# Kernel tuning notes

Hardware: AMD Instinct MI355X
Metric: run time of the kernel (lower is better)

Reference implementation:

```python
import jax, jax.numpy as jnp
import numpy as np

B, N, FDIM = 8, 2048, 256
ASSIGN_RATIO = 0.1
K = int(N * ASSIGN_RATIO) + 1  # num coarse nodes per graph (205)
DENSITY = 0.01


def setup_inputs() -> dict:
    key = jax.random.key(0)
    k1, k2, k3 = jax.random.split(key, 3)
    x = jax.random.normal(k1, (B, N, FDIM), dtype=jnp.float32)
    u = jax.random.uniform(k2, (B, N, N), dtype=jnp.float32)
    adj = jnp.where(u < DENSITY, u, 0.0)
    adj = 0.5 * (adj + jnp.swapaxes(adj, 1, 2))  # symmetric weighted adjacency
    W = jax.random.normal(k3, (FDIM, 1), dtype=jnp.float32) * 0.05
    b = jnp.zeros((1,), dtype=jnp.float32)
    return {"x": x, "adj": adj, "W": W, "b": b}


def _coarsen(x, adj, W, b):
    I = jnp.eye(N, dtype=adj.dtype)
    # --- GCNConv attention score (self-loops + symmetric normalization) ---
    A_hat = adj + I                       # [B,N,N]
    dg = A_hat.sum(-1) ** -0.5            # deg >= 1 via self-loop
    gcn_norm = dg[:, :, None] * A_hat * dg[:, None, :]
    alpha = jnp.einsum('bnm,bmf,fo->bno', gcn_norm, x, W) + b
    alpha = jax.nn.sigmoid(alpha ** 2)[..., 0]   # [B,N], sigmoid(gcn^2)
    # --- normalize_batch_adj: D^{-1/2}(A+I)D^{-1/2}, zero isolated rows ---
    d = jnp.clip(A_hat.sum(-1), 1.0, None) ** -0.5
    norm_adj = d[:, :, None] * A_hat * d[:, None, :]
    norm_adj = norm_adj * (adj.sum(-1) > 0).astype(adj.dtype)[:, :, None]
    # --- top-k cut on attention ---
    topv, topi = jax.lax.top_k(alpha, K)  # [B,K]
    cut = topv[:, K - 1]                  # k-th largest value per graph
    cut_alpha = jax.nn.relu(alpha + 1e-7 - cut[:, None])   # [B,N]
    # --- assignment matrix S = L1-row-normalized(norm_adj * cut_alpha_cols) ---
    S = norm_adj * cut_alpha[:, None, :]
    S = S / jnp.clip(jnp.abs(S).sum(-1, keepdims=True), 1e-12, None)
    # --- coarsening matmuls ---
    x_c = jnp.einsum('bnm,bnf->bmf', S, x)                 # S^T x
    coarse = jnp.einsum('bnm,bnk,bkl->bml', S, adj, S)     # S^T A S
    coarse = jnp.floor(coarse * 1e4) / 1e4                 # 4-digit truncation
    return x_c, coarse, S, topi


def reference(x, adj, W, b):
    return _coarsen(x, adj, W, b)
```

## Files before the change

kernel.cpp:

```cpp
#include <hip/hip_runtime.h>
#include <cstdint>
#include <cstddef>

#define BB 8
#define NN 2048
#define FD 256
#define KK 205
#define CAP 96
#define SELCAP 256

typedef float f4 __attribute__((ext_vector_type(4)));


__global__ __launch_bounds__(256) void k_spy(const float* __restrict__ adj, const float* __restrict__ x,
                                             const float* __restrict__ W, int2* __restrict__ ell,
                                             int* __restrict__ ell_cnt, float* __restrict__ dg,
                                             float* __restrict__ dgy) {
  int r = blockIdx.x;
  const f4* arow4 = (const f4*)(adj + (size_t)r * NN);
  int t = threadIdx.x;
  int lane = t & 63, wv = t >> 6;
  __shared__ int counter;
  __shared__ float wsum[4], wy[4];
  if (t == 0) counter = 0;
  __syncthreads();
  size_t base = (size_t)r * CAP;
  unsigned long long lmask = (1ull << lane) - 1;
  float ls = 0.f;
#pragma unroll
  for (int j = 0; j < 2; ++j) {
    int i4 = t + j * 256;
    f4 v = __builtin_nontemporal_load(&arow4[i4]);
    int m0 = i4 * 4;
#pragma unroll
    for (int c = 0; c < 4; ++c) {
      float val = v[c];
      unsigned long long mk = __ballot(val != 0.f);
      if (mk) {
        int wbase = 0;
        if (lane == 0) wbase = atomicAdd(&counter, (int)__popcll(mk));
        wbase = __shfl(wbase, 0);
        if (val != 0.f) {
          int p = wbase + (int)__popcll(mk & lmask);
          if (p < CAP) ell[base + p] = make_int2(m0 + c, __float_as_int(val));
        }
      }
      ls += val;
    }
  }
#pragma unroll
  for (int off = 32; off > 0; off >>= 1) ls += __shfl_down(ls, off);
  if (lane == 0) wsum[wv] = ls;
  float xv = x[(size_t)r * FD + t] * W[t];
#pragma unroll
  for (int off = 32; off > 0; off >>= 1) xv += __shfl_down(xv, off);
  if (lane == 0) wy[wv] = xv;
  __syncthreads();
  if (t == 0) {
    int tot = counter; if (tot > CAP) tot = CAP;
    ell_cnt[r] = tot;
    float rs = wsum[0] + wsum[1] + wsum[2] + wsum[3];
    float d = 1.0f / sqrtf(1.0f + rs);
    dg[r] = d;
    dgy[r] = d * (wy[0] + wy[1] + wy[2] + wy[3]);
  }
}

__global__ __launch_bounds__(256) void k_alpha(const int2* __restrict__ ell, const int* __restrict__ ell_cnt,
                                               const float* __restrict__ dg, const float* __restrict__ dgy,
                                               const float* __restrict__ bptr, float* __restrict__ alpha) {
  int lane = threadIdx.x & 63, wv = threadIdx.x >> 6;
  int r = blockIdx.x * 4 + wv;
  int b = r / NN;
  int cnt = ell_cnt[r];
  size_t base = (size_t)r * CAP;
  const float* gyb = dgy + (size_t)b * NN;
  float acc = 0.f;
  for (int j = lane; j < cnt; j += 64) {
    int2 e = ell[base + j];
    acc += __int_as_float(e.y) * gyb[e.x];
  }
#pragma unroll
  for (int off = 32; off > 0; off >>= 1) acc += __shfl_down(acc, off);
  if (lane == 0) {
    float dgn = dg[r];
    float z = dgn * (acc + dgy[r]) + bptr[0];
    float t2 = z * z;
    alpha[r] = 1.0f / (1.0f + expf(-t2));
  }
}

__global__ __launch_bounds__(256) void k_rank(const float* __restrict__ alpha, float* __restrict__ cutv,
                                              float* __restrict__ out_topi, int* __restrict__ sel_cnt) {
  __shared__ unsigned int keys[NN];
  int b = blockIdx.x & 7;
  int chunk = blockIdx.x >> 3;
  int t = threadIdx.x;
  if (chunk == 0 && t == 0) sel_cnt[b] = 0;
  const float* ab = alpha + (size_t)b * NN;
  for (int i = t; i < NN; i += 256) keys[i] = __float_as_uint(ab[i]);
  __syncthreads();
  int i = chunk * 256 + t;
  unsigned int ai = keys[i];
  int rank = 0;
  const uint4* k4 = (const uint4*)keys;
#pragma unroll 4
  for (int j4 = 0; j4 < NN / 4; ++j4) {
    uint4 v = k4[j4];
    int j = j4 * 4;
    rank += (v.x > ai) || (v.x == ai && (j + 0) < i);
    rank += (v.y > ai) || (v.y == ai && (j + 1) < i);
    rank += (v.z > ai) || (v.z == ai && (j + 2) < i);
    rank += (v.w > ai) || (v.w == ai && (j + 3) < i);
  }
  if (rank < KK) out_topi[(size_t)b * KK + rank] = (float)i;
  if (rank == KK - 1) cutv[b] = __uint_as_float(ai);
}

__global__ __launch_bounds__(256) void k_selcut(const float* __restrict__ alpha, const float* __restrict__ cutv,
                                                const float* __restrict__ dg, int2* __restrict__ seldg,
                                                int* __restrict__ sel_list, int* __restrict__ sel_cnt) {
  int r = blockIdx.x * 256 + threadIdx.x;
  int b = r / NN, n = r % NN;
  float ca = fmaxf(alpha[r] + 1e-7f - cutv[b], 0.0f);
  int s = -1;
  if (ca > 0.f) {
    s = atomicAdd(&sel_cnt[b], 1);
    if (s < SELCAP) sel_list[b * SELCAP + s] = n; else s = -1;
  }
  seldg[r] = make_int2(__float_as_int(dg[r] * ca), s);
}

__global__ __launch_bounds__(256) void k_sbuild(const int2* __restrict__ ell, const int* __restrict__ ell_cnt,
                                                const float* __restrict__ dg, const int2* __restrict__ seldg,
                                                const int* __restrict__ sel_cnt,
                                                float* __restrict__ dginv,
                                                float* __restrict__ Sc, float* __restrict__ outS) {
  __shared__ float row[NN];
  __shared__ float scrow[SELCAP];
  __shared__ int   sidx[CAP];
  __shared__ int   ssel[CAP];
  __shared__ float sterm[CAP];
  __shared__ float wred[4];
  int r = blockIdx.x;
  int b = r >> 11;
  int n = r & (NN - 1);
  int t = threadIdx.x;
  int lane = t & 63, wv = t >> 6;
#pragma unroll
  for (int j = 0; j < NN / 256; ++j) row[t + j * 256] = 0.f;
  if (t < SELCAP) scrow[t] = 0.f;
  int cnt = ell_cnt[r];
  size_t base = (size_t)r * CAP;
  float dgn = dg[r];
  const int2* sdb = seldg + (size_t)b * NN;
  float part = 0.f;
  for (int j = t; j < cnt; j += 256) {
    int2 e = ell[base + j];
    int2 sd = sdb[e.x];
    float term = dgn * __int_as_float(e.y) * __int_as_float(sd.x);
    sidx[j] = e.x; ssel[j] = sd.y; sterm[j] = term;
    part += term;
  }
#pragma unroll
  for (int off = 32; off > 0; off >>= 1) part += __shfl_down(part, off);
  if (lane == 0) wred[wv] = part;
  __syncthreads();
  int2 sdn = sdb[n];
  float diag = dgn * __int_as_float(sdn.x);
  float rho = wred[0] + wred[1] + wred[2] + wred[3] + diag;
  float inv = (cnt > 0) ? (1.0f / fmaxf(rho, 1e-12f)) : 0.f;
  float dv = diag * inv;
  if (t == 0) dginv[r] = dgn * inv;
  for (int j = t; j < cnt; j += 256) {
    float v = sterm[j] * inv;
    row[sidx[j]] = v;
    int si = ssel[j];
    if (si >= 0) scrow[si] = v;
  }
  __syncthreads();
  int nsel = sel_cnt[b]; if (nsel > SELCAP) nsel = SELCAP;
  f4* dst = (f4*)(outS + (size_t)r * NN);
  const f4* src = (const f4*)row;
#pragma unroll
  for (int j = 0; j < NN / 4 / 256; ++j) {
    int idx = t + j * 256;
    f4 v = src[idx];
    int b4 = idx * 4;
    v[0] += (b4 + 0 == n) ? dv : 0.f;
    v[1] += (b4 + 1 == n) ? dv : 0.f;
    v[2] += (b4 + 2 == n) ? dv : 0.f;
    v[3] += (b4 + 3 == n) ? dv : 0.f;
    __builtin_nontemporal_store(v, &dst[idx]);
  }
  if (t < nsel) {
    float sv = scrow[t];
    if (t == sdn.y) sv += dv;
    Sc[(size_t)r * SELCAP + t] = sv;
  }
}

__global__ __launch_bounds__(256) void k_M(const int2* __restrict__ ell, const int* __restrict__ ell_cnt,
                                           const int* __restrict__ sel_cnt,
                                           const float* __restrict__ Sc, float* __restrict__ Mmat) {
  int b = blockIdx.x & 7;
  int n = blockIdx.x >> 3;
  int r = b * NN + n;
  int t = threadIdx.x;
  __shared__ int srk[CAP];
  __shared__ float sav[CAP];
  int cnt = ell_cnt[r];
  size_t base = (size_t)r * CAP;
  for (int e = t; e < cnt; e += 256) {
    int2 p = ell[base + e];
    srk[e] = b * NN + p.x;
    sav[e] = __int_as_float(p.y);
  }
  __syncthreads();
  int nsel = sel_cnt[b]; if (nsel > SELCAP) nsel = SELCAP;
  if (t >= nsel) return;
  float a0 = 0.f, a1 = 0.f, a2 = 0.f, a3 = 0.f, a4 = 0.f, a5 = 0.f, a6 = 0.f, a7 = 0.f;
  int e = 0;
  for (; e + 8 <= cnt; e += 8) {
    a0 += sav[e + 0] * Sc[(size_t)srk[e + 0] * SELCAP + t];
    a1 += sav[e + 1] * Sc[(size_t)srk[e + 1] * SELCAP + t];
    a2 += sav[e + 2] * Sc[(size_t)srk[e + 2] * SELCAP + t];
    a3 += sav[e + 3] * Sc[(size_t)srk[e + 3] * SELCAP + t];
    a4 += sav[e + 4] * Sc[(size_t)srk[e + 4] * SELCAP + t];
    a5 += sav[e + 5] * Sc[(size_t)srk[e + 5] * SELCAP + t];
    a6 += sav[e + 6] * Sc[(size_t)srk[e + 6] * SELCAP + t];
    a7 += sav[e + 7] * Sc[(size_t)srk[e + 7] * SELCAP + t];
  }
  for (; e < cnt; ++e) a0 += sav[e] * Sc[(size_t)srk[e] * SELCAP + t];
  Mmat[(size_t)r * SELCAP + t] = ((a0 + a1) + (a2 + a3)) + ((a4 + a5) + (a6 + a7));
}

__global__ __launch_bounds__(256) void k_epi2(const float* __restrict__ x, const int2* __restrict__ ell,
                                              const int* __restrict__ ell_cnt, const int2* __restrict__ seldg,
                                              const float* __restrict__ dginv, const int* __restrict__ sel_list,
                                              const int* __restrict__ sel_cnt, const float* __restrict__ Mmat,
                                              float* __restrict__ xc, float* __restrict__ coarse) {
  int b = blockIdx.x & 7;
  int m = blockIdx.x >> 3;
  int rm = b * NN + m;
  int t = threadIdx.x;
  __shared__ float row[NN];
  __shared__ int cn[CAP + 1];
  __shared__ float cw[CAP + 1];
  int2 sd_m = seldg[rm];
  bool sel = sd_m.y >= 0;
  if (!sel) {
    f4 z = (f4)(0.f);
    if (t < FD / 4) __builtin_nontemporal_store(z, &((f4*)(xc + (size_t)rm * FD))[t]);
    f4* dco = (f4*)(coarse + (size_t)rm * NN);
    __builtin_nontemporal_store(z, &dco[t]);
    __builtin_nontemporal_store(z, &dco[t + 256]);
    return;
  }
  int nsel = sel_cnt[b]; if (nsel > SELCAP) nsel = SELCAP;
  int cnt = ell_cnt[rm];
#pragma unroll
  for (int j = 0; j < NN / 256; ++j) row[t + j * 256] = 0.f;
  {
    float dgca_m = __int_as_float(sd_m.x);
    for (int j = t; j <= cnt; j += 256) {
      if (j < cnt) {
        int2 e = ell[(size_t)rm * CAP + j];
        cn[j] = b * NN + e.x;
        cw[j] = __int_as_float(e.y) * dgca_m * dginv[b * NN + e.x];
      } else {
        cn[j] = rm;
        cw[j] = dgca_m * dginv[rm];
      }
    }
  }
  __syncthreads();
  bool act = t < nsel;
  float axc = 0.f, aco = 0.f;
  int tot = cnt + 1;
  int e = 0;
  for (; e + 4 <= tot; e += 4) {
    int r0 = cn[e + 0], r1 = cn[e + 1], r2 = cn[e + 2], r3 = cn[e + 3];
    float w0 = cw[e + 0], w1 = cw[e + 1], w2 = cw[e + 2], w3 = cw[e + 3];
    float x0 = x[(size_t)r0 * FD + t];
    float x1 = x[(size_t)r1 * FD + t];
    float x2 = x[(size_t)r2 * FD + t];
    float x3 = x[(size_t)r3 * FD + t];
    float m0 = 0.f, m1 = 0.f, m2 = 0.f, m3 = 0.f;
    if (act) {
      m0 = Mmat[(size_t)r0 * SELCAP + t];
      m1 = Mmat[(size_t)r1 * SELCAP + t];
      m2 = Mmat[(size_t)r2 * SELCAP + t];
      m3 = Mmat[(size_t)r3 * SELCAP + t];
    }
    axc += w0 * x0 + w1 * x1 + w2 * x2 + w3 * x3;
    aco += w0 * m0 + w1 * m1 + w2 * m2 + w3 * m3;
  }
  for (; e < tot; ++e) {
    int rn = cn[e];
    float w = cw[e];
    axc += w * x[(size_t)rn * FD + t];
    if (act) aco += w * Mmat[(size_t)rn * SELCAP + t];
  }
  if (act) row[sel_list[b * SELCAP + t]] = floorf(aco * 10000.0f) / 10000.0f;
  __builtin_nontemporal_store(axc, &xc[(size_t)rm * FD + t]);
  __syncthreads();
  f4* dst = (f4*)(coarse + (size_t)rm * NN);
  const f4* src = (const f4*)row;
#pragma unroll
  for (int j = 0; j < NN / 4 / 256; ++j)
    __builtin_nontemporal_store(src[t + j * 256], &dst[t + j * 256]);
}

extern "C" void kernel_launch(void* const* d_in, const int* in_sizes, int n_in,
                              void* d_out, int out_size, void* d_ws, size_t ws_size,
                              hipStream_t stream) {
  (void)in_sizes; (void)n_in; (void)ws_size; (void)out_size;
  const float* x = (const float*)d_in[0];
  const float* adj = (const float*)d_in[1];
  const float* W = (const float*)d_in[2];
  const float* bptr = (const float*)d_in[3];

  float* out = (float*)d_out;
  const size_t XC_SZ = (size_t)BB * NN * FD;
  const size_t CO_SZ = (size_t)BB * NN * NN;
  const size_t S_SZ  = (size_t)BB * NN * NN;
  float* out_xc = out;
  float* out_co = out + XC_SZ;
  float* out_S  = out + XC_SZ + CO_SZ;
  float* out_ti = out + XC_SZ + CO_SZ + S_SZ;

  char* w = (char*)d_ws;
  int2*  ell     = (int2*)w;  w += (size_t)BB * NN * CAP * 8;
  float* Sc      = (float*)w; w += (size_t)BB * NN * SELCAP * 4;
  float* Mmat    = (float*)w; w += (size_t)BB * NN * SELCAP * 4;
  int2*  seldg   = (int2*)w;  w += (size_t)BB * NN * 8;
  int*   ell_cnt = (int*)w;   w += (size_t)BB * NN * 4;
  float* dg      = (float*)w; w += (size_t)BB * NN * 4;
  float* dgy     = (float*)w; w += (size_t)BB * NN * 4;
  float* alpha   = (float*)w; w += (size_t)BB * NN * 4;
  float* dginv   = (float*)w; w += (size_t)BB * NN * 4;
  float* cutv    = (float*)w; w += (size_t)BB * 4;
  int*   sel_cnt = (int*)w;   w += (size_t)BB * 4;
  int*   sel_list= (int*)w;   w += (size_t)BB * SELCAP * 4;

  k_spy<<<BB * NN, 256, 0, stream>>>(adj, x, W, ell, ell_cnt, dg, dgy);
  k_alpha<<<BB * NN / 4, 256, 0, stream>>>(ell, ell_cnt, dg, dgy, bptr, alpha);
  k_rank<<<BB * 8, 256, 0, stream>>>(alpha, cutv, out_ti, sel_cnt);
  k_selcut<<<BB * NN / 256, 256, 0, stream>>>(alpha, cutv, dg, seldg, sel_list, sel_cnt);
  k_sbuild<<<BB * NN, 256, 0, stream>>>(ell, ell_cnt, dg, seldg, sel_cnt, dginv, Sc, out_S);
  k_M<<<BB * NN, 256, 0, stream>>>(ell, ell_cnt, sel_cnt, Sc, Mmat);
  k_epi2<<<BB * NN, 256, 0, stream>>>(x, ell, ell_cnt, seldg, dginv,
                                      sel_list, sel_cnt, Mmat, out_xc, out_co);
}
```

Baseline: 517.0 us.

## Split compact-S build into wave-per-row kernel and fuse dense S write into M kernel

The old S-build kernel did two jobs in one 256-thread block per row: building the compact selected-column row Sc and writing the dense 2048-wide S row. The new small kernel builds only Sc, with one wavefront per row and a shuffle reduction instead of block-wide barriers. The dense S write now happens inside the M kernel, which recomputes each row value from dginv and the ELL entries it already loads. This moves the heavy dense store so it overlaps with M's gather work and cuts barriers and launch width in the Sc build, at the cost of redundant ELL and seldg reads and the assumption that a row's nonzero count fits in 128.

```diff
diff --git a/kernel.cpp b/kernel.cpp
--- a/kernel.cpp
+++ b/kernel.cpp
@@ -131,55 +131,81 @@
   seldg[r] = make_int2(__float_as_int(dg[r] * ca), s);
 }
 
-__global__ __launch_bounds__(256) void k_sbuild(const int2* __restrict__ ell, const int* __restrict__ ell_cnt,
-                                                const float* __restrict__ dg, const int2* __restrict__ seldg,
-                                                const int* __restrict__ sel_cnt,
-                                                float* __restrict__ dginv,
-                                                float* __restrict__ Sc, float* __restrict__ outS) {
-  __shared__ float row[NN];
-  __shared__ float scrow[SELCAP];
-  __shared__ int   sidx[CAP];
-  __shared__ int   ssel[CAP];
-  __shared__ float sterm[CAP];
-  __shared__ float wred[4];
-  int r = blockIdx.x;
-  int b = r >> 11;
-  int n = r & (NN - 1);
-  int t = threadIdx.x;
-  int lane = t & 63, wv = t >> 6;
-#pragma unroll
-  for (int j = 0; j < NN / 256; ++j) row[t + j * 256] = 0.f;
-  if (t < SELCAP) scrow[t] = 0.f;
+__global__ __launch_bounds__(256) void k_sc(const int2* __restrict__ ell, const int* __restrict__ ell_cnt,
+                                            const float* __restrict__ dg, const int2* __restrict__ seldg,
+                                            const int* __restrict__ sel_cnt,
+                                            float* __restrict__ dginv, float* __restrict__ Sc) {
+  int lane = threadIdx.x & 63, wv = threadIdx.x >> 6;
+  int r = blockIdx.x * 4 + wv;
+  int b = r >> 11, n = r & (NN - 1);
+  __shared__ float scrow[4][SELCAP];
+  float* sc = scrow[wv];
+#pragma unroll
+  for (int j = lane; j < SELCAP; j += 64) sc[j] = 0.f;
   int cnt = ell_cnt[r];
   size_t base = (size_t)r * CAP;
   float dgn = dg[r];
   const int2* sdb = seldg + (size_t)b * NN;
-  float part = 0.f;
-  for (int j = t; j < cnt; j += 256) {
-    int2 e = ell[base + j];
+  float t0 = 0.f, t1 = 0.f;
+  int s0 = -1, s1 = -1;
+  if (lane < cnt) {
+    int2 e = ell[base + lane];
     int2 sd = sdb[e.x];
-    float term = dgn * __int_as_float(e.y) * __int_as_float(sd.x);
-    sidx[j] = e.x; ssel[j] = sd.y; sterm[j] = term;
-    part += term;
-  }
+    t0 = dgn * __int_as_float(e.y) * __int_as_float(sd.x);
+    s0 = sd.y;
+  }
+  if (lane + 64 < cnt) {
+    int2 e = ell[base + lane + 64];
+    int2 sd = sdb[e.x];
+    t1 = dgn * __int_as_float(e.y) * __int_as_float(sd.x);
+    s1 = sd.y;
+  }
+  float part = t0 + t1;
 #pragma unroll
   for (int off = 32; off > 0; off >>= 1) part += __shfl_down(part, off);
-  if (lane == 0) wred[wv] = part;
-  __syncthreads();
+  part = __shfl(part, 0);
   int2 sdn = sdb[n];
   float diag = dgn * __int_as_float(sdn.x);
-  float rho = wred[0] + wred[1] + wred[2] + wred[3] + diag;
+  float rho = part + diag;
   float inv = (cnt > 0) ? (1.0f / fmaxf(rho, 1e-12f)) : 0.f;
+  if (lane == 0) dginv[r] = dgn * inv;
+  if (s0 >= 0) sc[s0] = t0 * inv;
+  if (s1 >= 0) sc[s1] = t1 * inv;
+  int nsel = sel_cnt[b]; if (nsel > SELCAP) nsel = SELCAP;
   float dv = diag * inv;
-  if (t == 0) dginv[r] = dgn * inv;
-  for (int j = t; j < cnt; j += 256) {
-    float v = sterm[j] * inv;
-    row[sidx[j]] = v;
-    int si = ssel[j];
-    if (si >= 0) scrow[si] = v;
-  }
-  __syncthreads();
-  int nsel = sel_cnt[b]; if (nsel > SELCAP) nsel = SELCAP;
+  for (int p = lane; p < nsel; p += 64) {
+    float sv = sc[p];
+    if (p == sdn.y) sv += dv;
+    Sc[(size_t)r * SELCAP + p] = sv;
+  }
+}
+
+__global__ __launch_bounds__(256) void k_Ms(const int2* __restrict__ ell, const int* __restrict__ ell_cnt,
+                                            const int* __restrict__ sel_cnt, const int2* __restrict__ seldg,
+                                            const float* __restrict__ dginv, const float* __restrict__ Sc,
+                                            float* __restrict__ Mmat, float* __restrict__ outS) {
+  int b = blockIdx.x & 7;
+  int n = blockIdx.x >> 3;
+  int r = b * NN + n;
+  int t = threadIdx.x;
+  __shared__ float row[NN];
+  __shared__ int srk[CAP];
+  __shared__ float sav[CAP];
+#pragma unroll
+  for (int j = 0; j < NN / 256; ++j) row[t + j * 256] = 0.f;
+  int cnt = ell_cnt[r];
+  size_t base = (size_t)r * CAP;
+  float dinv = dginv[r];
+  const int2* sdb = seldg + (size_t)b * NN;
+  for (int e = t; e < cnt; e += 256) {
+    int2 p = ell[base + e];
+    srk[e] = b * NN + p.x;
+    float v = __int_as_float(p.y);
+    sav[e] = v;
+    row[p.x] = dinv * v * __int_as_float(sdb[p.x].x);
+  }
+  __syncthreads();
+  float dv = dinv * __int_as_float(sdb[n].x);
   f4* dst = (f4*)(outS + (size_t)r * NN);
   const f4* src = (const f4*)row;
 #pragma unroll
@@ -193,30 +219,6 @@
     v[3] += (b4 + 3 == n) ? dv : 0.f;
     __builtin_nontemporal_store(v, &dst[idx]);
   }
-  if (t < nsel) {
-    float sv = scrow[t];
-    if (t == sdn.y) sv += dv;
-    Sc[(size_t)r * SELCAP + t] = sv;
-  }
-}
-
-__global__ __launch_bounds__(256) void k_M(const int2* __restrict__ ell, const int* __restrict__ ell_cnt,
-                                           const int* __restrict__ sel_cnt,
-                                           const float* __restrict__ Sc, float* __restrict__ Mmat) {
-  int b = blockIdx.x & 7;
-  int n = blockIdx.x >> 3;
-  int r = b * NN + n;
-  int t = threadIdx.x;
-  __shared__ int srk[CAP];
-  __shared__ float sav[CAP];
-  int cnt = ell_cnt[r];
-  size_t base = (size_t)r * CAP;
-  for (int e = t; e < cnt; e += 256) {
-    int2 p = ell[base + e];
-    srk[e] = b * NN + p.x;
-    sav[e] = __int_as_float(p.y);
-  }
-  __syncthreads();
   int nsel = sel_cnt[b]; if (nsel > SELCAP) nsel = SELCAP;
   if (t >= nsel) return;
   float a0 = 0.f, a1 = 0.f, a2 = 0.f, a3 = 0.f, a4 = 0.f, a5 = 0.f, a6 = 0.f, a7 = 0.f;
@@ -348,8 +350,8 @@
   k_alpha<<<BB * NN / 4, 256, 0, stream>>>(ell, ell_cnt, dg, dgy, bptr, alpha);
   k_rank<<<BB * 8, 256, 0, stream>>>(alpha, cutv, out_ti, sel_cnt);
   k_selcut<<<BB * NN / 256, 256, 0, stream>>>(alpha, cutv, dg, seldg, sel_list, sel_cnt);
-  k_sbuild<<<BB * NN, 256, 0, stream>>>(ell, ell_cnt, dg, seldg, sel_cnt, dginv, Sc, out_S);
-  k_M<<<BB * NN, 256, 0, stream>>>(ell, ell_cnt, sel_cnt, Sc, Mmat);
+  k_sc<<<BB * NN / 4, 256, 0, stream>>>(ell, ell_cnt, dg, seldg, sel_cnt, dginv, Sc);
+  k_Ms<<<BB * NN, 256, 0, stream>>>(ell, ell_cnt, sel_cnt, seldg, dginv, Sc, Mmat, out_S);
   k_epi2<<<BB * NN, 256, 0, stream>>>(x, ell, ell_cnt, seldg, dginv,
                                       sel_list, sel_cnt, Mmat, out_xc, out_co);
 }
```

After: 506.2 us. 1.02x faster.
